# Optimization experiments

Measured on AMD Instinct MI355X. Metric: run time of the kernel, lower is better.

## Reference

```python
import jax, jax.numpy as jnp
import numpy as np

BAND_WIDTH = 0.5
EPS = 1e-5
NORM_EPS = 1e-12  # F.normalize eps


def setup_inputs() -> dict:
    key = jax.random.key(0)
    k1, k2 = jax.random.split(key)
    shape = (8, 512, 48, 48)  # N, C, H, W  (VGG conv4_4 features of a 384x384 image)
    return {
        "pred": jax.random.normal(k1, shape, dtype=jnp.float32),
        "target": jax.random.normal(k2, shape, dtype=jnp.float32),
    }


def reference(pred, target):
    N, C, H, W = pred.shape
    # center both by target channel-mean over (N, H, W)
    y_mu = jnp.mean(target, axis=(0, 2, 3), keepdims=True)
    x_c = pred - y_mu
    y_c = target - y_mu
    # L2-normalize along channel dim (F.normalize: divide by max(norm, eps))
    x_n = x_c / jnp.maximum(jnp.linalg.norm(x_c, axis=1, keepdims=True), NORM_EPS)
    y_n = y_c / jnp.maximum(jnp.linalg.norm(y_c, axis=1, keepdims=True), NORM_EPS)
    x_v = x_n.reshape(N, C, H * W)
    y_v = y_n.reshape(N, C, H * W)
    # pairwise cosine distance: [N, HW, HW]
    cosine_sim = jnp.einsum('ncp,ncq->npq', x_v, y_v)
    dist_raw = 1.0 - cosine_sim
    # relative distance: divide each row by its min over keys (dim=2)
    dist_min = jnp.min(dist_raw, axis=2, keepdims=True)
    dist_tilde = dist_raw / (dist_min + EPS)
    # similarity + row-normalize (softmax-like over dim=2)
    w = jnp.exp((1.0 - dist_tilde) / BAND_WIDTH)
    cx = w / jnp.sum(w, axis=2, keepdims=True)
    # max over query dim (dim=1), mean over key dim -> [N]
    cx = jnp.mean(jnp.max(cx, axis=1), axis=1)
    cx_loss = -jnp.log(cx + EPS)
    # reduction='mean', loss_weight=1.0
    return jnp.mean(cx_loss)
```

## Files before the change

### kernel.cpp

```cpp
#include <hip/hip_runtime.h>
#include <stdint.h>

#define NB 8
#define CC 512
#define PP 2304
#define EPSF 1e-5f
#define NPC 12
#define PCH 192

typedef short bf16x8 __attribute__((ext_vector_type(8)));
typedef float f32x4 __attribute__((ext_vector_type(4)));

typedef __attribute__((address_space(3))) uint8_t lds8_t;
typedef __attribute__((address_space(1))) const uint8_t g8_t;

__device__ __forceinline__ void async16(void* lds, const void* g) {
  __builtin_amdgcn_global_load_lds((g8_t*)g, (lds8_t*)lds, 16, 0, 0);
}

__device__ __forceinline__ float bf2f(uint32_t b16) {
  return __uint_as_float(b16 << 16);
}
__device__ __forceinline__ uint32_t f2bf(float f) {
  uint32_t u = __float_as_uint(f);
  return (u + 0x7fffu + ((u >> 16) & 1u)) >> 16;
}

__global__ __launch_bounds__(256) void k_chan_mean(const float* __restrict__ tgt,
                                                   float* __restrict__ mu) {
  const int c = blockIdx.x, t = threadIdx.x;
  float s = 0.f;
  for (int n = 0; n < NB; ++n) {
    const float* b = tgt + ((size_t)n * CC + c) * PP;
    for (int p = t; p < PP; p += 256) s += b[p];
  }
  for (int off = 32; off; off >>= 1) s += __shfl_down(s, off);
  __shared__ float red[4];
  if ((t & 63) == 0) red[t >> 6] = s;
  __syncthreads();
  if (t == 0) mu[c] = (red[0] + red[1] + red[2] + red[3]) * (1.0f / (NB * PP));
}

__global__ __launch_bounds__(256) void k_center_cast(
    const float* __restrict__ pred, const float* __restrict__ tgt,
    const float* __restrict__ mu,
    uint16_t* __restrict__ xt, uint16_t* __restrict__ yt,
    float* __restrict__ ssx, float* __restrict__ ssy) {
  __shared__ uint32_t lt[64][33];
  __shared__ float red[4][64];
  const int p0 = blockIdx.x * 64, c0 = blockIdx.y * 64, n = blockIdx.z;
  const int t = threadIdx.x, lp = t & 63, cb = t >> 6;
  for (int which = 0; which < 2; ++which) {
    const float* in = which ? tgt : pred;
    uint16_t* out = which ? yt : xt;
    float* ss = which ? ssy : ssx;
    float sq = 0.f;
    uint32_t packs[8];
#pragma unroll
    for (int i = 0; i < 16; ++i) {
      const int c = c0 + cb * 16 + i;
      float v = in[((size_t)n * CC + c) * PP + p0 + lp] - mu[c];
      sq += v * v;
      uint32_t b = f2bf(v);
      if (i & 1) packs[i >> 1] |= b << 16; else packs[i >> 1] = b;
    }
#pragma unroll
    for (int j = 0; j < 8; ++j) lt[lp][cb * 8 + j] = packs[j];
    red[cb][lp] = sq;
    __syncthreads();
    if (t < 64)
      atomicAdd(&ss[(size_t)n * PP + p0 + t],
                red[0][t] + red[1][t] + red[2][t] + red[3][t]);
    const int p = t >> 2, ch = t & 3;
    uint4 v0, v1;
    v0.x = lt[p][ch * 8 + 0]; v0.y = lt[p][ch * 8 + 1];
    v0.z = lt[p][ch * 8 + 2]; v0.w = lt[p][ch * 8 + 3];
    v1.x = lt[p][ch * 8 + 4]; v1.y = lt[p][ch * 8 + 5];
    v1.z = lt[p][ch * 8 + 6]; v1.w = lt[p][ch * 8 + 7];
    uint4* ob = (uint4*)(out + (((size_t)n * PP + p0 + p) * CC + c0 + ch * 16));
    ob[0] = v0; ob[1] = v1;
    __syncthreads();
  }
}

__global__ __launch_bounds__(256) void k_gemm(
    const uint16_t* __restrict__ xt, const uint16_t* __restrict__ yt,
    const float* __restrict__ ssx, const float* __restrict__ ssy,
    uint16_t* __restrict__ S) {
  __shared__ uint16_t As[128 * 64];
  __shared__ uint16_t Bs[128 * 64];
  int flat = blockIdx.x + 18 * blockIdx.y + 324 * blockIdx.z;
  flat = (flat & 7) * 324 + (flat >> 3);
  const int nb = flat / 324;
  const int rem = flat - nb * 324;
  const int byn = rem / 18;
  const int bxm = rem - byn * 18;
  const int m0 = bxm * 128, n0 = byn * 128;
  const int t = threadIdx.x, lane = t & 63, wid = t >> 6;
  const int wr = wid >> 1, wc = wid & 1;
  const uint16_t* Ax = xt + (size_t)nb * PP * CC;
  const uint16_t* By = yt + (size_t)nb * PP * CC;
  const int lrow = lane >> 3;
  const int lswz = (lane & 7) ^ lrow;
  const uint16_t* gA[4];
  const uint16_t* gB[4];
#pragma unroll
  for (int j = 0; j < 4; ++j) {
    const int row = (wid * 4 + j) * 8 + lrow;
    gA[j] = Ax + (size_t)(m0 + row) * CC + lswz * 8;
    gB[j] = By + (size_t)(n0 + row) * CC + lswz * 8;
  }
  f32x4 acc[4][4];
#pragma unroll
  for (int i = 0; i < 4; ++i)
#pragma unroll
    for (int j = 0; j < 4; ++j) acc[i][j] = (f32x4){0.f, 0.f, 0.f, 0.f};

  for (int k0 = 0; k0 < CC; k0 += 64) {
    __syncthreads();
#pragma unroll
    for (int j = 0; j < 4; ++j) {
      async16(As + (wid * 4 + j) * 512, gA[j] + k0);
      async16(Bs + (wid * 4 + j) * 512, gB[j] + k0);
    }
    __syncthreads();
#pragma unroll
    for (int kk = 0; kk < 2; ++kk) {
      const int kb = kk * 64 + (lane >> 4) * 16;
      bf16x8 af[4], bfr[4];
#pragma unroll
      for (int mi = 0; mi < 4; ++mi) {
        const int row = wr * 64 + mi * 16 + (lane & 15);
        af[mi] = *(const bf16x8*)((const char*)As + row * 128 + (kb ^ ((row & 7) << 4)));
      }
#pragma unroll
      for (int ni = 0; ni < 4; ++ni) {
        const int row = wc * 64 + ni * 16 + (lane & 15);
        bfr[ni] = *(const bf16x8*)((const char*)Bs + row * 128 + (kb ^ ((row & 7) << 4)));
      }
#pragma unroll
      for (int mi = 0; mi < 4; ++mi)
#pragma unroll
        for (int ni = 0; ni < 4; ++ni)
          acc[mi][ni] = __builtin_amdgcn_mfma_f32_16x16x32_bf16(
              af[mi], bfr[ni], acc[mi][ni], 0, 0, 0);
    }
  }
  const float* rsp = ssx + (size_t)nb * PP;
  const float* csp = ssy + (size_t)nb * PP;
  float rinv[4][4], cinv[4];
#pragma unroll
  for (int mi = 0; mi < 4; ++mi)
#pragma unroll
    for (int r = 0; r < 4; ++r)
      rinv[mi][r] = 1.0f / fmaxf(sqrtf(rsp[m0 + wr * 64 + mi * 16 + (lane >> 4) * 4 + r]), 1e-12f);
#pragma unroll
  for (int ni = 0; ni < 4; ++ni)
    cinv[ni] = 1.0f / fmaxf(sqrtf(csp[n0 + wc * 64 + ni * 16 + (lane & 15)]), 1e-12f);
  uint16_t* Sp = S + (size_t)nb * PP * PP;
#pragma unroll
  for (int mi = 0; mi < 4; ++mi) {
#pragma unroll
    for (int r = 0; r < 4; ++r) {
      const int grow = m0 + wr * 64 + mi * 16 + (lane >> 4) * 4 + r;
      uint16_t* rowp = Sp + (size_t)grow * PP + n0 + wc * 64 + (lane & 15);
#pragma unroll
      for (int ni = 0; ni < 4; ++ni) {
        float v = acc[mi][ni][r] * rinv[mi][r] * cinv[ni];
        rowp[ni * 16] = (uint16_t)f2bf(v);
      }
    }
  }
}

__global__ __launch_bounds__(256) void k_rowstats(const uint16_t* __restrict__ S,
                                                  float* __restrict__ dmin,
                                                  float* __restrict__ rsum) {
  const int row = blockIdx.x;
  const uint2* Sp = (const uint2*)(S + (size_t)row * PP);
  __shared__ __align__(16) float cosr[PP];
  __shared__ float reda[4], redb[4];
  const int t = threadIdx.x;
  float mx = -2.f;
  for (int i = t; i < PP / 4; i += 256) {
    uint2 u = Sp[i];
    float a = bf2f(u.x & 0xffffu), b = bf2f(u.x >> 16);
    float c = bf2f(u.y & 0xffffu), d = bf2f(u.y >> 16);
    *(float4*)&cosr[4 * i] = make_float4(a, b, c, d);
    mx = fmaxf(fmaxf(mx, fmaxf(a, b)), fmaxf(c, d));
  }
  for (int off = 32; off; off >>= 1) mx = fmaxf(mx, __shfl_down(mx, off));
  if ((t & 63) == 0) reda[t >> 6] = mx;
  __syncthreads();
  mx = fmaxf(fmaxf(reda[0], reda[1]), fmaxf(reda[2], reda[3]));
  const float dm = 1.0f - mx;
  const float sc = 2.0f / (dm + EPSF);
  float s = 0.f;
  for (int i = t; i < PP; i += 256) s += __expf((cosr[i] - mx + EPSF) * sc);
  for (int off = 32; off; off >>= 1) s += __shfl_down(s, off);
  if ((t & 63) == 0) redb[t >> 6] = s;
  __syncthreads();
  if (t == 0) { dmin[row] = dm; rsum[row] = redb[0] + redb[1] + redb[2] + redb[3]; }
}

__global__ __launch_bounds__(256) void k_colmax_part(const uint16_t* __restrict__ S,
                                                     const float* __restrict__ dmin,
                                                     const float* __restrict__ rsum,
                                                     float* __restrict__ pcm) {
  const int n = blockIdx.y, pc = blockIdx.z, t = threadIdx.x;
  const int q2 = blockIdx.x * 512 + 2 * t;
  __shared__ float lmx[PCH], lsc[PCH], lri[PCH];
  const float* dmn = dmin + (size_t)n * PP + pc * PCH;
  const float* rsn = rsum + (size_t)n * PP + pc * PCH;
  for (int i = t; i < PCH; i += 256) {
    float dm = dmn[i];
    lmx[i] = 1.0f - dm - EPSF;
    lsc[i] = 2.0f / (dm + EPSF);
    lri[i] = 1.0f / rsn[i];
  }
  __syncthreads();
  if (q2 >= PP) return;
  const uint32_t* Sn =
      (const uint32_t*)(S + (size_t)n * PP * PP + (size_t)pc * PCH * PP + q2);
  float b0 = 0.f, b1 = 0.f;
#pragma unroll 8
  for (int p = 0; p < PCH; ++p) {
    uint32_t u = Sn[(size_t)p * (PP / 2)];
    float mxv = lmx[p], scv = lsc[p], riv = lri[p];
    b0 = fmaxf(b0, __expf((bf2f(u & 0xffffu) - mxv) * scv) * riv);
    b1 = fmaxf(b1, __expf((bf2f(u >> 16) - mxv) * scv) * riv);
  }
  float* o = pcm + ((size_t)n * NPC + pc) * PP + q2;
  o[0] = b0; o[1] = b1;
}

__global__ __launch_bounds__(256) void k_colmax_fin(const float* __restrict__ pcm,
                                                    float* __restrict__ cxacc) {
  const int n = blockIdx.y, t = threadIdx.x;
  const int q = blockIdx.x * 256 + t;
  float best = 0.f;
#pragma unroll
  for (int c = 0; c < NPC; ++c) best = fmaxf(best, pcm[((size_t)n * NPC + c) * PP + q]);
  float s = best;
  for (int off = 32; off; off >>= 1) s += __shfl_down(s, off);
  __shared__ float red[4];
  if ((t & 63) == 0) red[t >> 6] = s;
  __syncthreads();
  if (t == 0) atomicAdd(&cxacc[n], red[0] + red[1] + red[2] + red[3]);
}

__global__ void k_final(const float* __restrict__ cxacc, float* __restrict__ out) {
  if (threadIdx.x == 0 && blockIdx.x == 0) {
    float s = 0.f;
    for (int n = 0; n < NB; ++n) {
      float cx = cxacc[n] * (1.0f / PP);
      s += -logf(cx + EPSF);
    }
    out[0] = s * (1.0f / NB);
  }
}

extern "C" void kernel_launch(void* const* d_in, const int* in_sizes, int n_in,
                              void* d_out, int out_size, void* d_ws, size_t ws_size,
                              hipStream_t stream) {
  const float* pred = (const float*)d_in[0];
  const float* tgt  = (const float*)d_in[1];
  float* W = (float*)d_ws;
  float* mu   = W + 0;
  float* ssx  = W + 1024;
  float* ssy  = W + 19456;
  float* cx   = W + 37888;
  float* dmin = W + 75264;
  float* rsum = W + 93696;
  uint16_t* xt = (uint16_t*)(W + 223744);
  uint16_t* yt = xt + (size_t)NB * PP * CC;
  uint16_t* S  = yt + (size_t)NB * PP * CC;
  float* pcm = (float*)xt;

  hipMemsetAsync(W + 1024, 0, (36872) * sizeof(float), stream);

  k_chan_mean<<<dim3(CC), dim3(256), 0, stream>>>(tgt, mu);
  k_center_cast<<<dim3(PP / 64, CC / 64, NB), dim3(256), 0, stream>>>(
      pred, tgt, mu, xt, yt, ssx, ssy);
  k_gemm<<<dim3(PP / 128, PP / 128, NB), dim3(256), 0, stream>>>(xt, yt, ssx, ssy, S);
  k_rowstats<<<dim3(NB * PP), dim3(256), 0, stream>>>(S, dmin, rsum);
  k_colmax_part<<<dim3((PP + 511) / 512, NB, NPC), dim3(256), 0, stream>>>(
      S, dmin, rsum, pcm);
  k_colmax_fin<<<dim3(PP / 256, NB), dim3(256), 0, stream>>>(pcm, cx);
  k_final<<<1, 64, 0, stream>>>(cx, (float*)d_out);
}
```

Before: 170.7 us.

## Rewrite similarity GEMM as 256x256 tile, 8-wave, double-buffered pipelined kernel

Replaces the 128x128, 4-wave GEMM, which loaded and then synchronised on every K step, with a 256x256 tile computed by 8 waves. LDS is double-buffered in quadrants and the next K slice is staged asynchronously while MFMAs run on the current one. Explicit vmcnt waits, raw barriers and setprio control the overlap. The larger tile raises data reuse and hides global latency, at the cost of 128KB of LDS per block, fewer blocks (648), fragile hand-tuned wait counts and a less balanced tail.

```diff
diff --git a/kernel.cpp b/kernel.cpp
--- a/kernel.cpp
+++ b/kernel.cpp
@@ -24,6 +24,14 @@
 __device__ __forceinline__ uint32_t f2bf(float f) {
   uint32_t u = __float_as_uint(f);
   return (u + 0x7fffu + ((u >> 16) & 1u)) >> 16;
+}
+
+template <int N>
+__device__ __forceinline__ void vmwait() {
+  if constexpr (N == 0) asm volatile("s_waitcnt vmcnt(0)" ::: "memory");
+  else if constexpr (N == 4) asm volatile("s_waitcnt vmcnt(4)" ::: "memory");
+  else if constexpr (N == 6) asm volatile("s_waitcnt vmcnt(6)" ::: "memory");
+  else if constexpr (N == 8) asm volatile("s_waitcnt vmcnt(8)" ::: "memory");
 }
 
 __global__ __launch_bounds__(256) void k_chan_mean(const float* __restrict__ tgt,
@@ -83,94 +91,145 @@
   }
 }
 
-__global__ __launch_bounds__(256) void k_gemm(
+
+__device__ __forceinline__ void stage_half(uint16_t* reg, const uint16_t* g, int tid) {
+  async16((char*)reg + tid * 16, g);
+  async16((char*)reg + tid * 16 + 8192, g + 64 * CC);
+}
+
+template <int QM, int QN, bool LOADA, bool STG, int VM>
+__device__ __forceinline__ void phase(const uint16_t (*R)[8192],
+                                      uint16_t* sdst, const uint16_t* ssrc,
+                                      int tid, int lane, int wr, int wcn,
+                                      bf16x8 (&af)[4][2], f32x4 (&acc)[2][4][2][2]) {
+  if (LOADA) {
+#pragma unroll
+    for (int i = 0; i < 4; ++i) {
+      const int rh = wr * 64 + i * 16 + (lane & 15);
+      const char* base = (const char*)R[QM] + rh * 128;
+      const int sw = (rh & 7) << 4;
+#pragma unroll
+      for (int kk = 0; kk < 2; ++kk)
+        af[i][kk] = *(const bf16x8*)(base + ((kk * 64 + (lane >> 4) * 16) ^ sw));
+    }
+  }
+  bf16x8 bf[2][2];
+#pragma unroll
+  for (int j = 0; j < 2; ++j) {
+    const int rh = wcn * 32 + j * 16 + (lane & 15);
+    const char* base = (const char*)R[2 + QN] + rh * 128;
+    const int sw = (rh & 7) << 4;
+#pragma unroll
+    for (int kk = 0; kk < 2; ++kk)
+      bf[j][kk] = *(const bf16x8*)(base + ((kk * 64 + (lane >> 4) * 16) ^ sw));
+  }
+  if (STG) stage_half(sdst, ssrc, tid);
+  __builtin_amdgcn_s_barrier();
+  asm volatile("s_waitcnt lgkmcnt(0)" ::: "memory");
+  __builtin_amdgcn_s_setprio(1);
+#pragma unroll
+  for (int i = 0; i < 4; ++i)
+#pragma unroll
+    for (int j = 0; j < 2; ++j)
+#pragma unroll
+      for (int kk = 0; kk < 2; ++kk)
+        acc[QM][i][QN][j] = __builtin_amdgcn_mfma_f32_16x16x32_bf16(
+            af[i][kk], bf[j][kk], acc[QM][i][QN][j], 0, 0, 0);
+  __builtin_amdgcn_s_setprio(0);
+  vmwait<VM>();
+  __builtin_amdgcn_s_barrier();
+}
+
+__global__ __launch_bounds__(512, 2) void k_gemm(
     const uint16_t* __restrict__ xt, const uint16_t* __restrict__ yt,
     const float* __restrict__ ssx, const float* __restrict__ ssy,
     uint16_t* __restrict__ S) {
-  __shared__ uint16_t As[128 * 64];
-  __shared__ uint16_t Bs[128 * 64];
-  int flat = blockIdx.x + 18 * blockIdx.y + 324 * blockIdx.z;
-  flat = (flat & 7) * 324 + (flat >> 3);
-  const int nb = flat / 324;
-  const int rem = flat - nb * 324;
-  const int byn = rem / 18;
-  const int bxm = rem - byn * 18;
-  const int m0 = bxm * 128, n0 = byn * 128;
-  const int t = threadIdx.x, lane = t & 63, wid = t >> 6;
-  const int wr = wid >> 1, wc = wid & 1;
+  __shared__ uint16_t lds[2][4][8192];
+  int flat = blockIdx.x + 9 * blockIdx.y + 81 * blockIdx.z;
+  flat = (flat & 7) * 81 + (flat >> 3);
+  const int nb = flat / 81;
+  const int rem = flat - nb * 81;
+  const int m0 = (rem % 9) * 256, n0 = (rem / 9) * 256;
+  const int tid = threadIdx.x, lane = tid & 63, wid = tid >> 6;
+  const int wr = wid >> 2, wcn = wid & 3;
   const uint16_t* Ax = xt + (size_t)nb * PP * CC;
   const uint16_t* By = yt + (size_t)nb * PP * CC;
-  const int lrow = lane >> 3;
-  const int lswz = (lane & 7) ^ lrow;
-  const uint16_t* gA[4];
-  const uint16_t* gB[4];
-#pragma unroll
-  for (int j = 0; j < 4; ++j) {
-    const int row = (wid * 4 + j) * 8 + lrow;
-    gA[j] = Ax + (size_t)(m0 + row) * CC + lswz * 8;
-    gB[j] = By + (size_t)(n0 + row) * CC + lswz * 8;
-  }
-  f32x4 acc[4][4];
-#pragma unroll
-  for (int i = 0; i < 4; ++i)
-#pragma unroll
-    for (int j = 0; j < 4; ++j) acc[i][j] = (f32x4){0.f, 0.f, 0.f, 0.f};
-
-  for (int k0 = 0; k0 < CC; k0 += 64) {
-    __syncthreads();
-#pragma unroll
-    for (int j = 0; j < 4; ++j) {
-      async16(As + (wid * 4 + j) * 512, gA[j] + k0);
-      async16(Bs + (wid * 4 + j) * 512, gB[j] + k0);
-    }
-    __syncthreads();
-#pragma unroll
-    for (int kk = 0; kk < 2; ++kk) {
-      const int kb = kk * 64 + (lane >> 4) * 16;
-      bf16x8 af[4], bfr[4];
-#pragma unroll
-      for (int mi = 0; mi < 4; ++mi) {
-        const int row = wr * 64 + mi * 16 + (lane & 15);
-        af[mi] = *(const bf16x8*)((const char*)As + row * 128 + (kb ^ ((row & 7) << 4)));
+  const int lswz = (tid & 7) ^ ((tid >> 3) & 7);
+  const uint16_t* gAb = Ax + (size_t)(m0 + (tid >> 3)) * CC + lswz * 8;
+  const uint16_t* gBb = By + (size_t)(n0 + (tid >> 3)) * CC + lswz * 8;
+
+  f32x4 acc[2][4][2][2];
+#pragma unroll
+  for (int a = 0; a < 2; ++a)
+#pragma unroll
+    for (int b = 0; b < 4; ++b)
+#pragma unroll
+      for (int c = 0; c < 2; ++c)
+#pragma unroll
+        for (int d = 0; d < 2; ++d) acc[a][b][c][d] = (f32x4){0.f, 0.f, 0.f, 0.f};
+
+  stage_half(lds[0][0], gAb, tid);
+  stage_half(lds[0][2], gBb, tid);
+  stage_half(lds[0][1], gAb + 128 * CC, tid);
+  stage_half(lds[0][3], gBb + 128 * CC, tid);
+  stage_half(lds[1][0], gAb + 64, tid);
+  stage_half(lds[1][2], gBb + 64, tid);
+  vmwait<8>();
+  __builtin_amdgcn_s_barrier();
+
+  bf16x8 af[4][2];
+  for (int kt = 0; kt < 6; ++kt) {
+    const int cur = kt & 1;
+    const uint16_t(*R)[8192] = lds[cur];
+    uint16_t(*Wn)[8192] = lds[cur ^ 1];
+    uint16_t(*Wc)[8192] = lds[cur];
+    const int ko = (kt + 1) * 64;
+    phase<0, 0, true, true, 6>(R, Wn[1], gAb + 128 * CC + ko, tid, lane, wr, wcn, af, acc);
+    phase<0, 1, false, true, -1>(R, Wn[3], gBb + 128 * CC + ko, tid, lane, wr, wcn, af, acc);
+    phase<1, 0, true, true, -1>(R, Wc[0], gAb + ko + 64, tid, lane, wr, wcn, af, acc);
+    phase<1, 1, false, true, 8>(R, Wc[2], gBb + ko + 64, tid, lane, wr, wcn, af, acc);
+  }
+  {
+    const uint16_t(*R)[8192] = lds[0];
+    phase<0, 0, true, true, 6>(R, lds[1][1], gAb + 128 * CC + 7 * 64, tid, lane, wr, wcn, af, acc);
+    phase<0, 1, false, true, -1>(R, lds[1][3], gBb + 128 * CC + 7 * 64, tid, lane, wr, wcn, af, acc);
+    phase<1, 0, true, false, -1>(R, nullptr, nullptr, tid, lane, wr, wcn, af, acc);
+    phase<1, 1, false, false, 4>(R, nullptr, nullptr, tid, lane, wr, wcn, af, acc);
+  }
+  {
+    const uint16_t(*R)[8192] = lds[1];
+    phase<0, 0, true, false, 0>(R, nullptr, nullptr, tid, lane, wr, wcn, af, acc);
+    phase<0, 1, false, false, -1>(R, nullptr, nullptr, tid, lane, wr, wcn, af, acc);
+    phase<1, 0, true, false, -1>(R, nullptr, nullptr, tid, lane, wr, wcn, af, acc);
+    phase<1, 1, false, false, -1>(R, nullptr, nullptr, tid, lane, wr, wcn, af, acc);
+  }
+
+  const float* rsp = ssx + (size_t)nb * PP + m0;
+  const float* csp = ssy + (size_t)nb * PP + n0;
+  uint16_t* Sp = S + (size_t)nb * PP * PP;
+  float cinv[2][2];
+#pragma unroll
+  for (int qn = 0; qn < 2; ++qn)
+#pragma unroll
+    for (int j = 0; j < 2; ++j)
+      cinv[qn][j] =
+          1.0f / fmaxf(sqrtf(csp[qn * 128 + wcn * 32 + j * 16 + (lane & 15)]), 1e-12f);
+#pragma unroll
+  for (int qm = 0; qm < 2; ++qm)
+#pragma unroll
+    for (int i = 0; i < 4; ++i)
+#pragma unroll
+      for (int r = 0; r < 4; ++r) {
+        const int row = qm * 128 + wr * 64 + i * 16 + (lane >> 4) * 4 + r;
+        const float ri = 1.0f / fmaxf(sqrtf(rsp[row]), 1e-12f);
+        uint16_t* orow = Sp + (size_t)(m0 + row) * PP + n0;
+#pragma unroll
+        for (int qn = 0; qn < 2; ++qn)
+#pragma unroll
+          for (int j = 0; j < 2; ++j)
+            orow[qn * 128 + wcn * 32 + j * 16 + (lane & 15)] =
+                (uint16_t)f2bf(acc[qm][i][qn][j][r] * ri * cinv[qn][j]);
       }
-#pragma unroll
-      for (int ni = 0; ni < 4; ++ni) {
-        const int row = wc * 64 + ni * 16 + (lane & 15);
-        bfr[ni] = *(const bf16x8*)((const char*)Bs + row * 128 + (kb ^ ((row & 7) << 4)));
-      }
-#pragma unroll
-      for (int mi = 0; mi < 4; ++mi)
-#pragma unroll
-        for (int ni = 0; ni < 4; ++ni)
-          acc[mi][ni] = __builtin_amdgcn_mfma_f32_16x16x32_bf16(
-              af[mi], bfr[ni], acc[mi][ni], 0, 0, 0);
-    }
-  }
-  const float* rsp = ssx + (size_t)nb * PP;
-  const float* csp = ssy + (size_t)nb * PP;
-  float rinv[4][4], cinv[4];
-#pragma unroll
-  for (int mi = 0; mi < 4; ++mi)
-#pragma unroll
-    for (int r = 0; r < 4; ++r)
-      rinv[mi][r] = 1.0f / fmaxf(sqrtf(rsp[m0 + wr * 64 + mi * 16 + (lane >> 4) * 4 + r]), 1e-12f);
-#pragma unroll
-  for (int ni = 0; ni < 4; ++ni)
-    cinv[ni] = 1.0f / fmaxf(sqrtf(csp[n0 + wc * 64 + ni * 16 + (lane & 15)]), 1e-12f);
-  uint16_t* Sp = S + (size_t)nb * PP * PP;
-#pragma unroll
-  for (int mi = 0; mi < 4; ++mi) {
-#pragma unroll
-    for (int r = 0; r < 4; ++r) {
-      const int grow = m0 + wr * 64 + mi * 16 + (lane >> 4) * 4 + r;
-      uint16_t* rowp = Sp + (size_t)grow * PP + n0 + wc * 64 + (lane & 15);
-#pragma unroll
-      for (int ni = 0; ni < 4; ++ni) {
-        float v = acc[mi][ni][r] * rinv[mi][r] * cinv[ni];
-        rowp[ni * 16] = (uint16_t)f2bf(v);
-      }
-    }
-  }
 }
 
 __global__ __launch_bounds__(256) void k_rowstats(const uint16_t* __restrict__ S,
@@ -282,7 +341,7 @@
   k_chan_mean<<<dim3(CC), dim3(256), 0, stream>>>(tgt, mu);
   k_center_cast<<<dim3(PP / 64, CC / 64, NB), dim3(256), 0, stream>>>(
       pred, tgt, mu, xt, yt, ssx, ssy);
-  k_gemm<<<dim3(PP / 128, PP / 128, NB), dim3(256), 0, stream>>>(xt, yt, ssx, ssy, S);
+  k_gemm<<<dim3(9, 9, NB), dim3(512), 0, stream>>>(xt, yt, ssx, ssy, S);
   k_rowstats<<<dim3(NB * PP), dim3(256), 0, stream>>>(S, dmin, rsum);
   k_colmax_part<<<dim3((PP + 511) / 512, NB, NPC), dim3(256), 0, stream>>>(
       S, dmin, rsum, pcm);
```

Result: faster. 159.7 us (-6.4%).
